# Performance work log

Hardware: AMD Instinct MI355X
Metric: run time of the kernel (lower is better)

The kernel has to match this reference:

```python
import jax, jax.numpy as jnp
import numpy as np

B, F, H, W = 1, 4, 20, 44
P = H * W            # 880 tokens per frame (20*44, from max_attention_size = 15*880)
S = F * P            # 3520 packed tokens
DIM, NH, FFN, OUT = 1536, 12, 6144, 64   # OUT = prod(patch_size)*out_dim = 4*16
HD = DIM // NH       # 128
C = HD // 2          # 64 rotary complex pairs
EPS = 1e-6


def _rope_angles():
    # Wan 3D RoPE: split C pairs as (C-2*(C//3), C//3, C//3) over (frame, h, w)
    cf, ch, cw = C - 2 * (C // 3), C // 3, C // 3
    def tab(n, cp):
        inv = 1.0 / (10000.0 ** (np.arange(cp) / cp))
        return np.outer(np.arange(n), inv)
    af = np.broadcast_to(tab(F, cf)[:, None, None, :], (F, H, W, cf))
    ah = np.broadcast_to(tab(H, ch)[None, :, None, :], (F, H, W, ch))
    aw = np.broadcast_to(tab(W, cw)[None, None, :, :], (F, H, W, cw))
    return np.concatenate([af, ah, aw], -1).reshape(S, C).astype(np.float32)


def setup_inputs() -> dict:
    key = jax.random.key(0)
    ks = jax.random.split(key, 24)
    g = lambda i, shape, s=0.02: jax.random.normal(ks[i], shape, dtype=jnp.float32) * s
    inp = {
        'x': jax.random.normal(ks[0], (B, S, DIM), dtype=jnp.float32),
        'e': g(1, (B, F, 6, DIM), 1.0),
        'e_head': g(2, (B, F, 2, DIM), 1.0),
        'rope_angles': jnp.asarray(_rope_angles()),
        'mod_block': g(3, (1, 6, DIM), 1.0 / float(np.sqrt(DIM))),
        'mod_head': g(4, (1, 2, DIM), 1.0 / float(np.sqrt(DIM))),
        'Wq': g(5, (DIM, DIM)), 'bq': jnp.zeros((DIM,), jnp.float32),
        'Wk': g(6, (DIM, DIM)), 'bk': jnp.zeros((DIM,), jnp.float32),
        'Wv': g(7, (DIM, DIM)), 'bv': jnp.zeros((DIM,), jnp.float32),
        'Wo': g(8, (DIM, DIM)), 'bo': jnp.zeros((DIM,), jnp.float32),
        'wq_norm': jnp.ones((DIM,), jnp.float32),
        'wk_norm': jnp.ones((DIM,), jnp.float32),
        'W1': g(9, (DIM, FFN)), 'b1': jnp.zeros((FFN,), jnp.float32),
        'W2': g(10, (FFN, DIM)), 'b2': jnp.zeros((DIM,), jnp.float32),
        'Wh': g(11, (DIM, OUT)), 'bh': jnp.zeros((OUT,), jnp.float32),
    }
    return inp


def _ln(x):
    # WanLayerNorm without elementwise affine
    m = jnp.mean(x, axis=-1, keepdims=True)
    v = jnp.var(x, axis=-1, keepdims=True)
    return (x - m) * jax.lax.rsqrt(v + EPS)


def _rms(x, w):
    return x * jax.lax.rsqrt(jnp.mean(x * x, axis=-1, keepdims=True) + EPS) * w


def _rope(t, ang):
    # t: [B,S,NH,HD]; adjacent pairs form complex numbers (view_as_complex style)
    tr = t.reshape(B, S, NH, C, 2)
    cos = jnp.cos(ang)[None, :, None, :]
    sin = jnp.sin(ang)[None, :, None, :]
    t0, t1 = tr[..., 0], tr[..., 1]
    return jnp.stack([t0 * cos - t1 * sin, t0 * sin + t1 * cos], -1).reshape(B, S, NH, HD)


def reference(x, e, e_head, rope_angles, mod_block, mod_head,
              Wq, bq, Wk, bk, Wv, bv, Wo, bo, wq_norm, wk_norm,
              W1, b1, W2, b2, Wh, bh):
    # ---- AdaLN modulation split (6-way) ----
    em = mod_block[:, None] + e                      # [B,F,6,DIM]
    e0, e1, e2, e3, e4, e5 = [em[:, :, i][:, :, None, :] for i in range(6)]

    xf = x.reshape(B, F, P, DIM)
    h = (_ln(xf) * (1 + e1) + e0).reshape(B, S, DIM)

    # ---- QK-RMSNorm + RoPE self attention (block-causal, block = one frame) ----
    q = _rope(_rms(h @ Wq + bq, wq_norm).reshape(B, S, NH, HD), rope_angles)
    k = _rope(_rms(h @ Wk + bk, wk_norm).reshape(B, S, NH, HD), rope_angles)
    v = (h @ Wv + bv).reshape(B, S, NH, HD)

    blk = jnp.arange(S) // P
    mask = blk[None, :] <= blk[:, None]              # [S,S] block-causal
    scores = jnp.einsum('bqhd,bkhd->bhqk', q, k) / np.float32(np.sqrt(HD))
    scores = jnp.where(mask[None, None], scores, jnp.float32(-1e30))
    attn = jax.nn.softmax(scores, axis=-1)
    y = jnp.einsum('bhqk,bkhd->bqhd', attn, v).reshape(B, S, DIM) @ Wo + bo

    xf = xf + y.reshape(B, F, P, DIM) * e2

    # ---- FFN with AdaLN modulation ----
    hf = (_ln(xf) * (1 + e4) + e3).reshape(B, S, DIM)
    ff = jax.nn.gelu(hf @ W1 + b1) @ W2 + b2
    xf = xf + ff.reshape(B, F, P, DIM) * e5

    # ---- OutputHead: modulated norm + linear ----
    eh = mod_head[:, None] + e_head                  # [B,F,2,DIM]
    eh0 = eh[:, :, 0][:, :, None, :]
    eh1 = eh[:, :, 1][:, :, None, :]
    out = (_ln(xf) * (1 + eh1) + eh0) @ Wh + bh      # [B,F,P,OUT]
    return out
```

## Files before the change

kernel.cpp:

```cpp
#include <hip/hip_runtime.h>
#include <cstdint>
#include <cstddef>

typedef __bf16 bf16;
typedef __bf16 bf16x2 __attribute__((ext_vector_type(2)));
typedef __bf16 bf16x8 __attribute__((ext_vector_type(8)));
typedef float f32x4 __attribute__((ext_vector_type(4)));
typedef unsigned int u32x4 __attribute__((ext_vector_type(4)));

#define S_TOK 3520
#define S_PAD 3584
#define P_TOK 880
#define NFRM 4
#define DIM 1536
#define NH 12
#define HD 128
#define FFN_D 6144
#define NOUT 64
#define EPSV 1e-6f
#define QSCALE 0.12751743f

__device__ __forceinline__ f32x4 mfma16(bf16x8 a, bf16x8 b, f32x4 c) {
  return __builtin_amdgcn_mfma_f32_16x16x32_bf16(a, b, c, 0, 0, 0);
}

__device__ __forceinline__ void gload_lds16(const bf16* g, bf16* l) {
  __builtin_amdgcn_global_load_lds(
      (const __attribute__((address_space(1))) unsigned int*)g,
      (__attribute__((address_space(3))) unsigned int*)l, 16, 0, 0);
}

__device__ __forceinline__ uint32_t pk2(float lo, float hi) {
  bf16x2 t;
  t[0] = (bf16)lo;
  t[1] = (bf16)hi;
  return __builtin_bit_cast(uint32_t, t);
}

__global__ __launch_bounds__(256) void k_prep(const float* __restrict__ e,
                                              const float* __restrict__ e_head,
                                              const float* __restrict__ mod_block,
                                              const float* __restrict__ mod_head,
                                              float* __restrict__ em,
                                              float* __restrict__ ehm) {
  int i = blockIdx.x * 256 + threadIdx.x;
  if (i < NFRM * 6 * DIM) em[i] = mod_block[i % (6 * DIM)] + e[i];
  int j = i - NFRM * 6 * DIM;
  if (j >= 0 && j < NFRM * 2 * DIM) ehm[j] = mod_head[j % (2 * DIM)] + e_head[j];
}

__global__ __launch_bounds__(256) void k_zero_vpad(bf16* __restrict__ vc) {
  size_t base = ((size_t)blockIdx.x * 28 + 27) * 4096 + 2048 + (size_t)threadIdx.x * 8;
#pragma unroll
  for (int i = 0; i < 8; ++i) vc[base + i] = (bf16)0.f;
}

__global__ __launch_bounds__(256) void k_transpose(const float* __restrict__ W,
                                                   bf16* __restrict__ Wt, int K, int N) {
  __shared__ float tile[32][33];
  int n0 = blockIdx.x * 32, k0 = blockIdx.y * 32;
  int tx = threadIdx.x & 31, ty = threadIdx.x >> 5;
#pragma unroll
  for (int j = 0; j < 4; ++j) {
    int k = k0 + ty * 4 + j;
    float v = (n0 + tx < N) ? W[(size_t)k * N + n0 + tx] : 0.f;
    tile[ty * 4 + j][tx] = v;
  }
  __syncthreads();
#pragma unroll
  for (int j = 0; j < 4; ++j) {
    int n = n0 + ty * 4 + j;
    if (n < N) Wt[(size_t)n * K + k0 + tx] = (bf16)tile[tx][ty * 4 + j];
  }
}

__global__ __launch_bounds__(256) void k_adaln(const float* __restrict__ in,
                                               bf16* __restrict__ out,
                                               const float* __restrict__ e_shift,
                                               const float* __restrict__ e_scale,
                                               int fstride) {
  int tok = blockIdx.x;
  int t = threadIdx.x;
  bf16* orow = out + (size_t)tok * DIM;
  if (tok >= S_TOK) {
#pragma unroll
    for (int i = 0; i < 6; ++i) orow[t * 6 + i] = (bf16)0.f;
    return;
  }
  const float* xrow = in + (size_t)tok * DIM;
  float v[6];
  float s = 0.f, sq = 0.f;
#pragma unroll
  for (int i = 0; i < 6; ++i) {
    v[i] = xrow[t * 6 + i];
    s += v[i];
    sq += v[i] * v[i];
  }
  for (int off = 32; off; off >>= 1) {
    s += __shfl_down(s, off);
    sq += __shfl_down(sq, off);
  }
  __shared__ float red[8];
  int wv = t >> 6, lane = t & 63;
  if (lane == 0) { red[wv] = s; red[4 + wv] = sq; }
  __syncthreads();
  float ts = red[0] + red[1] + red[2] + red[3];
  float tq = red[4] + red[5] + red[6] + red[7];
  float mean = ts * (1.f / DIM);
  float var = tq * (1.f / DIM) - mean * mean;
  float rstd = rsqrtf(var + EPSV);
  int f = tok / P_TOK;
  const float* sh = e_shift + (size_t)f * fstride;
  const float* sc = e_scale + (size_t)f * fstride;
#pragma unroll
  for (int i = 0; i < 6; ++i) {
    int d = t * 6 + i;
    orow[d] = (bf16)((v[i] - mean) * rstd * (1.f + sc[d]) + sh[d]);
  }
}

__global__ __launch_bounds__(256) void k_qkv_post(const float* __restrict__ qkv,
                                                  const float* __restrict__ wqn,
                                                  const float* __restrict__ wkn,
                                                  const float* __restrict__ ang,
                                                  bf16* __restrict__ qb,
                                                  bf16* __restrict__ kb,
                                                  bf16* __restrict__ vc) {
  int s = blockIdx.x;
  int t = threadIdx.x;
  const float* row = qkv + (size_t)s * 3 * DIM;
  float qv[6], kv[6], vv[6];
  float sqq = 0.f, sqk = 0.f;
  int d0 = t * 6;
#pragma unroll
  for (int i = 0; i < 6; ++i) {
    int d = d0 + i;
    qv[i] = row[d];
    kv[i] = row[DIM + d];
    vv[i] = row[2 * DIM + d];
    sqq += qv[i] * qv[i];
    sqk += kv[i] * kv[i];
  }
  float a1 = sqq, a2 = sqk;
  for (int off = 32; off; off >>= 1) {
    a1 += __shfl_down(a1, off);
    a2 += __shfl_down(a2, off);
  }
  __shared__ float red[8];
  int wv = t >> 6, lane = t & 63;
  if (lane == 0) { red[wv] = a1; red[4 + wv] = a2; }
  __syncthreads();
  float tq = red[0] + red[1] + red[2] + red[3];
  float tk = red[4] + red[5] + red[6] + red[7];
  float rq = rsqrtf(tq * (1.f / DIM) + EPSV);
  float rk = rsqrtf(tk * (1.f / DIM) + EPSV);
#pragma unroll
  for (int p = 0; p < 3; ++p) {
    int d = d0 + p * 2;
    int h = d >> 7;
    int hd = d & 127;
    int c = hd >> 1;
    float a = ang[(size_t)s * 64 + c];
    float sa, ca;
    sincosf(a, &sa, &ca);
    float q0 = qv[p * 2] * rq * wqn[d], q1 = qv[p * 2 + 1] * rq * wqn[d + 1];
    float k0 = kv[p * 2] * rk * wkn[d], k1 = kv[p * 2 + 1] * rk * wkn[d + 1];
    size_t base = ((size_t)h * S_TOK + s) * HD + hd;
    qb[base]     = (bf16)((q0 * ca - q1 * sa) * QSCALE);
    qb[base + 1] = (bf16)((q0 * sa + q1 * ca) * QSCALE);
    kb[base]     = (bf16)(k0 * ca - k1 * sa);
    kb[base + 1] = (bf16)(k0 * sa + k1 * ca);
  }
  int f = s / P_TOK;
  int l = s - f * P_TOK;
  int lb = l >> 5, gg = (l >> 3) & 3, r = l & 7;
#pragma unroll
  for (int i = 0; i < 6; ++i) {
    int d = d0 + i;
    int h = d >> 7, hd = d & 127;
    vc[((((size_t)(h * NFRM + f)) * 28 + lb) * 512 + gg * 128 + hd) * 8 + r] = (bf16)vv[i];
  }
}

__global__ __launch_bounds__(320) void k_attn(const bf16* __restrict__ qb,
                                              const bf16* __restrict__ kb,
                                              const bf16* __restrict__ vc,
                                              float* __restrict__ parto,
                                              float* __restrict__ partml) {
  __shared__ __align__(16) bf16 Ks[2][512 * 8];
  __shared__ __align__(16) bf16 Vs[2][512 * 8];
  int h = blockIdx.x / 110;
  int p = blockIdx.x % 110;
  int f = (p < 11) ? 0 : (p < 33) ? 1 : (p < 66) ? 2 : 3;
  int cum = (f == 0) ? 0 : (f == 1) ? 11 : (f == 2) ? 33 : 66;
  int w = p - cum;
  int kc = w / 11;
  int qt = f * 11 + w % 11;
  int slot = blockIdx.x;
  int t = threadIdx.x;
  int wv = t >> 6, lane = t & 63;
  int r16 = lane & 15, g = lane >> 4;
  int q0 = qt * 80 + wv * 16;
  int kv0 = kc * P_TOK;
  const bf16* qbase = qb + ((size_t)h * S_TOK + q0 + r16) * HD + g * 8;
  bf16x8 qf[4];
#pragma unroll
  for (int kk = 0; kk < 4; ++kk) qf[kk] = *(const bf16x8*)(qbase + kk * 32);
  f32x4 acc[8] = {};
  float mrow = -1e30f, lrow = 0.f;
  int src01 = r16 + ((2 * g) & 3) * 16;
  int src23 = src01 + 16;
  bool glo = (g < 2);
  int sB = t + 256;
  int kr0 = t >> 4, kl0 = t & 15;
  int ks0 = (kl0 & 8) | ((kl0 ^ kr0) & 7);
  int kr1 = sB >> 4, kl1 = sB & 15;
  int ks1 = (kl1 & 8) | ((kl1 ^ kr1) & 7);
  const bf16* kh = kb + (size_t)h * S_TOK * HD;
  const bf16* vchunk = vc + ((size_t)(h * NFRM + kc)) * 28 * 4096;
#define STAGE_ATT(buf, jj)                                                  \
  do {                                                                      \
    int kvoj = (jj) * 32;                                                   \
    int gr0 = kv0 + kvoj + kr0; if (gr0 >= S_TOK) gr0 = 0;                  \
    int gr1 = kv0 + kvoj + kr1; if (gr1 >= S_TOK) gr1 = 0;                  \
    gload_lds16(kh + (size_t)gr0 * HD + ks0 * 8, Ks[buf] + t * 8);          \
    gload_lds16(kh + (size_t)gr1 * HD + ks1 * 8, Ks[buf] + sB * 8);         \
    gload_lds16(vchunk + (size_t)(jj) * 4096 + t * 8, Vs[buf] + t * 8);     \
    gload_lds16(vchunk + (size_t)(jj) * 4096 + sB * 8, Vs[buf] + sB * 8);   \
  } while (0)
  const int nsteps = (P_TOK + 31) >> 5;
  if (t < 256) STAGE_ATT(0, 0);
  int cur = 0;
  for (int j = 0; j < nsteps; ++j) {
    int kvo = j * 32;
    if (j + 1 < nsteps) {
      if (t < 256) STAGE_ATT(cur ^ 1, j + 1);
      asm volatile("s_waitcnt vmcnt(4)" ::: "memory");
    } else {
      asm volatile("s_waitcnt vmcnt(0)" ::: "memory");
    }
    __builtin_amdgcn_s_barrier();
    f32x4 st0 = {0.f, 0.f, 0.f, 0.f}, st1 = {0.f, 0.f, 0.f, 0.f};
#pragma unroll
    for (int kk = 0; kk < 4; ++kk) {
      int sl = g + 4 * kk;
      int ss = (sl & 8) | ((sl ^ r16) & 7);
      bf16x8 k0 = *(const bf16x8*)(Ks[cur] + (r16 * 16 + ss) * 8);
      bf16x8 k1 = *(const bf16x8*)(Ks[cur] + ((16 + r16) * 16 + ss) * 8);
      st0 = mfma16(k0, qf[kk], st0);
      st1 = mfma16(k1, qf[kk], st1);
    }
    float hm = (kvo + 16 >= P_TOK) ? -1e30f : 0.f;
    float a0[4], a1[4];
#pragma unroll
    for (int r = 0; r < 4; ++r) {
      a0[r] = st0[r];
      a1[r] = st1[r] + hm;
    }
    float tm = fmaxf(fmaxf(fmaxf(a0[0], a0[1]), fmaxf(a0[2], a0[3])),
                     fmaxf(fmaxf(a1[0], a1[1]), fmaxf(a1[2], a1[3])));
    tm = fmaxf(tm, __shfl_xor(tm, 16));
    tm = fmaxf(tm, __shfl_xor(tm, 32));
    float mn = fmaxf(mrow, tm);
    float p0[4], p1[4], ps = 0.f;
#pragma unroll
    for (int r = 0; r < 4; ++r) {
      p0[r] = exp2f(a0[r] - mn);
      p1[r] = exp2f(a1[r] - mn);
      ps += p0[r] + p1[r];
    }
    float scl = exp2f(mrow - mn);
    mrow = mn;
    lrow = lrow * scl + ps;
    uint32_t A0 = pk2(p0[0], p0[1]), A1 = pk2(p0[2], p0[3]);
    uint32_t B0 = pk2(p1[0], p1[1]), B1 = pk2(p1[2], p1[3]);
    uint32_t sA0 = __shfl(A0, src01), sA1 = __shfl(A1, src01);
    uint32_t sB0 = __shfl(B0, src01), sB1 = __shfl(B1, src01);
    uint32_t tA0 = __shfl(A0, src23), tA1 = __shfl(A1, src23);
    uint32_t tB0 = __shfl(B0, src23), tB1 = __shfl(B1, src23);
    u32x4 wds;
    wds[0] = glo ? sA0 : sB0;
    wds[1] = glo ? sA1 : sB1;
    wds[2] = glo ? tA0 : tB0;
    wds[3] = glo ? tA1 : tB1;
    bf16x8 pb = __builtin_bit_cast(bf16x8, wds);
#pragma unroll
    for (int hb = 0; hb < 8; ++hb) {
      acc[hb][0] *= scl;
      acc[hb][1] *= scl;
      acc[hb][2] *= scl;
      acc[hb][3] *= scl;
    }
    const bf16* vsl = Vs[cur] + (size_t)(g * 128 + r16) * 8;
#pragma unroll
    for (int hb = 0; hb < 8; ++hb) {
      bf16x8 vfr = *(const bf16x8*)(vsl + hb * 128);
      acc[hb] = mfma16(vfr, pb, acc[hb]);
    }
    asm volatile("" ::: "memory");
    __builtin_amdgcn_s_barrier();
    cur ^= 1;
  }
#undef STAGE_ATT
  lrow += __shfl_xor(lrow, 16);
  lrow += __shfl_xor(lrow, 32);
  float* obase = parto + (((size_t)slot * 5 + wv) * 8) * 256;
#pragma unroll
  for (int hb = 0; hb < 8; ++hb) {
    *(f32x4*)(obase + (hb * 64 + lane) * 4) = acc[hb];
  }
  if (g == 0) {
    float* mlb = partml + ((size_t)slot * 5 + wv) * 32;
    mlb[r16] = mrow;
    mlb[16 + r16] = lrow;
  }
}

__global__ __launch_bounds__(256) void k_att_reduce(const float* __restrict__ parto,
                                                    const float* __restrict__ partml,
                                                    bf16* __restrict__ attb) {
  int b = blockIdx.x;
  int h = b / 44, qt = b % 44;
  int f = qt / 11, j = qt % 11;
  int cum = (f == 0) ? 0 : (f == 1) ? 11 : (f == 2) ? 33 : 66;
  int t = threadIdx.x;
  int d = t & 127, half = t >> 7;
  int hb = d >> 4, g = (d >> 2) & 3, r = d & 3;
  int q0 = qt * 80;
  for (int it = 0; it < 40; ++it) {
    int qloc = it + 40 * half;
    int wv = qloc >> 4, r16 = qloc & 15;
    float m[4], l[4];
    float mt = -1e30f;
    for (int kc = 0; kc <= f; ++kc) {
      int slot = h * 110 + cum + kc * 11 + j;
      const float* mlb = partml + ((size_t)slot * 5 + wv) * 32;
      m[kc] = mlb[r16];
      l[kc] = mlb[16 + r16];
      mt = fmaxf(mt, m[kc]);
    }
    float lt = 0.f, o = 0.f;
    for (int kc = 0; kc <= f; ++kc) {
      int slot = h * 110 + cum + kc * 11 + j;
      float wgt = exp2f(m[kc] - mt);
      lt += l[kc] * wgt;
      o += parto[(((size_t)slot * 5 + wv) * 8 + hb) * 256 + (g * 16 + r16) * 4 + r] * wgt;
    }
    attb[(size_t)(q0 + qloc) * DIM + h * HD + d] = (bf16)(o / lt);
  }
}

struct GemmP {
  const bf16* A;
  const bf16* Bt;
  int K;
  int Mtiles;
  int Ntiles;
  int Mreal;
  int mode;
  const float* bias0;
  const float* bias1;
  const float* bias2;
  const float* res;
  const float* emod;
  int e_fstride;
  float* outf;
  bf16* outb;
  int ldo;
};

__global__ __launch_bounds__(256, 3) void k_gemm(GemmP p) {
  int nwg = p.Mtiles * p.Ntiles;
  int bid = blockIdx.x;
  int l = bid;
  if ((nwg & 7) == 0) {
    int cpx = nwg >> 3;
    l = (bid & 7) * cpx + (bid >> 3);
  }
  int bm = l % p.Mtiles;
  int bn = l / p.Mtiles;
  __shared__ __align__(16) bf16 As[3][128 * 32];
  __shared__ __align__(16) bf16 Bs[3][128 * 32];
  int t = threadIdx.x, lane = t & 63, wv = t >> 6;
  int r16 = lane & 15, g = lane >> 4;
  int wr = wv >> 1, wc = wv & 1;
  f32x4 acc[4][4] = {};
  const bf16* Ag = p.A + (size_t)bm * 128 * p.K;
  const bf16* Bg = p.Bt + (size_t)bn * 128 * p.K;
  int c0 = t, c1 = t + 256;
  int row0 = c0 >> 2, off0 = (c0 & 3) * 8;
  int row1 = c1 >> 2, off1 = (c1 & 3) * 8;
#define STAGE(buf, kk)                                                     \
  do {                                                                     \
    gload_lds16(Ag + (size_t)row0 * p.K + (kk) + off0, As[buf] + c0 * 8);  \
    gload_lds16(Ag + (size_t)row1 * p.K + (kk) + off1, As[buf] + c1 * 8);  \
    gload_lds16(Bg + (size_t)row0 * p.K + (kk) + off0, Bs[buf] + c0 * 8);  \
    gload_lds16(Bg + (size_t)row1 * p.K + (kk) + off1, Bs[buf] + c1 * 8);  \
  } while (0)
  const int nt = p.K >> 5;
  STAGE(0, 0);
  STAGE(1, 32);
  int cur = 0;
  for (int tt = 0; tt < nt; ++tt) {
    int rem = nt - 1 - tt;
    if (rem >= 2) {
      int nb = cur + 2;
      if (nb >= 3) nb -= 3;
      STAGE(nb, (tt + 2) * 32);
      asm volatile("s_waitcnt vmcnt(8)" ::: "memory");
    } else if (rem == 1) {
      asm volatile("s_waitcnt vmcnt(4)" ::: "memory");
    } else {
      asm volatile("s_waitcnt vmcnt(0)" ::: "memory");
    }
    __builtin_amdgcn_s_barrier();
    bf16x8 af[4], bfr[4];
#pragma unroll
    for (int mi = 0; mi < 4; ++mi)
      af[mi] = *(const bf16x8*)(As[cur] + (wr * 64 + mi * 16 + r16) * 32 + g * 8);
#pragma unroll
    for (int ni = 0; ni < 4; ++ni)
      bfr[ni] = *(const bf16x8*)(Bs[cur] + (wc * 64 + ni * 16 + r16) * 32 + g * 8);
#pragma unroll
    for (int mi = 0; mi < 4; ++mi)
#pragma unroll
      for (int ni = 0; ni < 4; ++ni)
        acc[mi][ni] = mfma16(af[mi], bfr[ni], acc[mi][ni]);
    asm volatile("" ::: "memory");
    __builtin_amdgcn_s_barrier();
    cur = (cur + 1 == 3) ? 0 : cur + 1;
  }
#undef STAGE
  int mb = bm * 128 + wr * 64, nb0 = bn * 128 + wc * 64;
#pragma unroll
  for (int mi = 0; mi < 4; ++mi) {
#pragma unroll
    for (int ni = 0; ni < 4; ++ni) {
      int col = nb0 + ni * 16 + r16;
#pragma unroll
      for (int r = 0; r < 4; ++r) {
        int row = mb + mi * 16 + 4 * g + r;
        if (row >= p.Mreal) continue;
        float v = acc[mi][ni][r];
        if (p.mode == 0) {
          float b = col < DIM ? p.bias0[col]
                              : (col < 2 * DIM ? p.bias1[col - DIM] : p.bias2[col - 2 * DIM]);
          p.outf[(size_t)row * p.ldo + col] = v + b;
        } else if (p.mode == 1) {
          int fr = row / P_TOK;
          p.outf[(size_t)row * p.ldo + col] =
              p.res[(size_t)row * DIM + col] +
              (v + p.bias0[col]) * p.emod[(size_t)fr * p.e_fstride + col];
        } else if (p.mode == 2) {
          float xg = v + p.bias0[col];
          float gl = 0.5f * xg * (1.f + tanhf(0.7978845608028654f * (xg + 0.044715f * xg * xg * xg)));
          p.outb[(size_t)row * p.ldo + col] = (bf16)gl;
        } else {
          if (col < NOUT) p.outf[(size_t)row * p.ldo + col] = v + p.bias0[col];
        }
      }
    }
  }
}

extern "C" void kernel_launch(void* const* d_in, const int* in_sizes, int n_in,
                              void* d_out, int out_size, void* d_ws, size_t ws_size,
                              hipStream_t stream) {
  const float* x = (const float*)d_in[0];
  const float* e = (const float*)d_in[1];
  const float* e_head = (const float*)d_in[2];
  const float* ang = (const float*)d_in[3];
  const float* mod_block = (const float*)d_in[4];
  const float* mod_head = (const float*)d_in[5];
  const float* Wq = (const float*)d_in[6];
  const float* bq = (const float*)d_in[7];
  const float* Wk = (const float*)d_in[8];
  const float* bk = (const float*)d_in[9];
  const float* Wv = (const float*)d_in[10];
  const float* bv = (const float*)d_in[11];
  const float* Wo = (const float*)d_in[12];
  const float* bo = (const float*)d_in[13];
  const float* wqn = (const float*)d_in[14];
  const float* wkn = (const float*)d_in[15];
  const float* W1 = (const float*)d_in[16];
  const float* b1 = (const float*)d_in[17];
  const float* W2 = (const float*)d_in[18];
  const float* b2 = (const float*)d_in[19];
  const float* Wh = (const float*)d_in[20];
  const float* bh = (const float*)d_in[21];
  float* out = (float*)d_out;
  char* ws = (char*)d_ws;

  size_t WT_QKV = 0;
  size_t WT_O = WT_QKV + (size_t)3 * DIM * DIM * 2;
  size_t W1T = WT_O + (size_t)DIM * DIM * 2;
  size_t W2T = W1T + (size_t)FFN_D * DIM * 2;
  size_t WHT = W2T + (size_t)DIM * FFN_D * 2;
  size_t EMOFF = WHT + (size_t)128 * DIM * 2;
  size_t EHOFF = EMOFF + (size_t)NFRM * 6 * DIM * 4;
  size_t HB = EHOFF + (size_t)NFRM * 2 * DIM * 4;
  size_t CQKV = HB + (size_t)S_PAD * DIM * 2;
  size_t DQB = CQKV + (size_t)S_TOK * 3 * DIM * 4;
  size_t EATT = DQB + (size_t)3 * NH * S_TOK * HD * 2;
  size_t GXF2 = EATT + (size_t)S_PAD * DIM * 2;
  size_t END = GXF2 + (size_t)S_TOK * DIM * 4;
  if (ws_size < END) return;

  bf16* wtqkv = (bf16*)(ws + WT_QKV);
  bf16* wto = (bf16*)(ws + WT_O);
  bf16* w1t = (bf16*)(ws + W1T);
  bf16* w2t = (bf16*)(ws + W2T);
  bf16* wht = (bf16*)(ws + WHT);
  float* em = (float*)(ws + EMOFF);
  float* ehm = (float*)(ws + EHOFF);
  bf16* hb = (bf16*)(ws + HB);
  float* qkvf = (float*)(ws + CQKV);
  bf16* ffb = (bf16*)(ws + CQKV);
  float* parto = (float*)(ws + CQKV);
  float* partml = parto + (size_t)1320 * 5 * 8 * 256;
  bf16* qbp = (bf16*)(ws + DQB);
  bf16* kbp = qbp + (size_t)NH * S_TOK * HD;
  bf16* vcp = kbp + (size_t)NH * S_TOK * HD;
  float* xf3 = (float*)(ws + DQB);
  bf16* attb = (bf16*)(ws + EATT);
  float* xf2 = (float*)(ws + GXF2);

  k_prep<<<(NFRM * 8 * DIM) / 256, 256, 0, stream>>>(e, e_head, mod_block, mod_head, em, ehm);
  k_zero_vpad<<<NH * NFRM, 256, 0, stream>>>(vcp);

  k_transpose<<<dim3(48, 48), 256, 0, stream>>>(Wq, wtqkv, DIM, DIM);
  k_transpose<<<dim3(48, 48), 256, 0, stream>>>(Wk, wtqkv + (size_t)DIM * DIM, DIM, DIM);
  k_transpose<<<dim3(48, 48), 256, 0, stream>>>(Wv, wtqkv + (size_t)2 * DIM * DIM, DIM, DIM);
  k_transpose<<<dim3(48, 48), 256, 0, stream>>>(Wo, wto, DIM, DIM);
  k_transpose<<<dim3(192, 48), 256, 0, stream>>>(W1, w1t, DIM, FFN_D);
  k_transpose<<<dim3(48, 192), 256, 0, stream>>>(W2, w2t, FFN_D, DIM);
  k_transpose<<<dim3(2, 48), 256, 0, stream>>>(Wh, wht, DIM, NOUT);
  hipMemsetAsync(ws + WHT + (size_t)NOUT * DIM * 2, 0, (size_t)(128 - NOUT) * DIM * 2, stream);
  hipMemsetAsync(ws + EATT + (size_t)S_TOK * DIM * 2, 0, (size_t)(S_PAD - S_TOK) * DIM * 2, stream);

  k_adaln<<<S_PAD, 256, 0, stream>>>(x, hb, em, em + DIM, 6 * DIM);

  GemmP g0{};
  g0.A = hb; g0.Bt = wtqkv; g0.K = DIM; g0.Mtiles = 28; g0.Ntiles = 36; g0.Mreal = S_TOK;
  g0.mode = 0; g0.bias0 = bq; g0.bias1 = bk; g0.bias2 = bv; g0.outf = qkvf; g0.ldo = 3 * DIM;
  k_gemm<<<28 * 36, 256, 0, stream>>>(g0);

  k_qkv_post<<<S_TOK, 256, 0, stream>>>(qkvf, wqn, wkn, ang, qbp, kbp, vcp);

  k_attn<<<NH * 110, 320, 0, stream>>>(qbp, kbp, vcp, parto, partml);
  k_att_reduce<<<NH * 44, 256, 0, stream>>>(parto, partml, attb);

  GemmP g1{};
  g1.A = attb; g1.Bt = wto; g1.K = DIM; g1.Mtiles = 28; g1.Ntiles = 12; g1.Mreal = S_TOK;
  g1.mode = 1; g1.bias0 = bo; g1.res = x; g1.emod = em + 2 * DIM; g1.e_fstride = 6 * DIM;
  g1.outf = xf2; g1.ldo = DIM;
  k_gemm<<<28 * 12, 256, 0, stream>>>(g1);

  k_adaln<<<S_PAD, 256, 0, stream>>>(xf2, hb, em + 3 * DIM, em + 4 * DIM, 6 * DIM);

  GemmP g2{};
  g2.A = hb; g2.Bt = w1t; g2.K = DIM; g2.Mtiles = 28; g2.Ntiles = 48; g2.Mreal = S_TOK;
  g2.mode = 2; g2.bias0 = b1; g2.outb = ffb; g2.ldo = FFN_D;
  k_gemm<<<28 * 48, 256, 0, stream>>>(g2);
  hipMemsetAsync(ws + CQKV + (size_t)S_TOK * FFN_D * 2, 0, (size_t)(S_PAD - S_TOK) * FFN_D * 2, stream);

  GemmP g3{};
  g3.A = ffb; g3.Bt = w2t; g3.K = FFN_D; g3.Mtiles = 28; g3.Ntiles = 12; g3.Mreal = S_TOK;
  g3.mode = 1; g3.bias0 = b2; g3.res = xf2; g3.emod = em + 5 * DIM; g3.e_fstride = 6 * DIM;
  g3.outf = xf3; g3.ldo = DIM;
  k_gemm<<<28 * 12, 256, 0, stream>>>(g3);

  k_adaln<<<S_PAD, 256, 0, stream>>>(xf3, hb, ehm, ehm + DIM, 2 * DIM);

  GemmP g4{};
  g4.A = hb; g4.Bt = wht; g4.K = DIM; g4.Mtiles = 28; g4.Ntiles = 1; g4.Mreal = S_TOK;
  g4.mode = 4; g4.bias0 = bh; g4.outf = out; g4.ldo = NOUT;
  k_gemm<<<28, 256, 0, stream>>>(g4);
}
```

Measured before the change: 803.0 us.

## Use 256x256-tile 512-thread GEMM kernel for QKV and FFN-up projections

Adds a new GEMM kernel with 256x256 output tiles, 8 waves per block, double-buffered swizzled LDS staging, XCD-aware block remapping and MFMA priority hints. It is used for the QKV projection and the first FFN matmul with GELU in place of the 128-tile kernel. The larger tiles raise arithmetic intensity and cut global reloads of A and B. In exchange it uses 128KB of LDS, which limits blocks per CU, and fewer blocks (252 and 336) may leave CUs underused or give wave-quantization tails.

```diff
diff --git a/kernel.cpp b/kernel.cpp
--- a/kernel.cpp
+++ b/kernel.cpp
@@ -347,6 +347,124 @@
       o += parto[(((size_t)slot * 5 + wv) * 8 + hb) * 256 + (g * 16 + r16) * 4 + r] * wgt;
     }
     attb[(size_t)(q0 + qloc) * DIM + h * HD + d] = (bf16)(o / lt);
+  }
+}
+
+struct Gemm256P {
+  const bf16* A;
+  const bf16* Bt;
+  int K;
+  int Mtiles;
+  int Ntiles;
+  int Mreal;
+  int mode;
+  const float* bias0;
+  const float* bias1;
+  const float* bias2;
+  float* outf;
+  bf16* outb;
+  int ldo;
+};
+
+__global__ __launch_bounds__(512, 2) void k_gemm256(Gemm256P p) {
+  int nwg = p.Mtiles * p.Ntiles;
+  int bid = blockIdx.x;
+  int xq = nwg >> 3, xr = nwg & 7;
+  int xcd = bid & 7, jj = bid >> 3;
+  int wg = (xcd < xr ? xcd * (xq + 1) : xr * (xq + 1) + (xcd - xr) * xq) + jj;
+  int bm = wg % p.Mtiles;
+  int bn = wg / p.Mtiles;
+  __shared__ __align__(16) bf16 Asl[2][256 * 64];
+  __shared__ __align__(16) bf16 Bsl[2][256 * 64];
+  int t = threadIdx.x, lane = t & 63, wv = t >> 6;
+  int r16 = lane & 15, g = lane >> 4;
+  int wr = wv >> 2, wc = wv & 3;
+  f32x4 acc[8][4] = {};
+  const bf16* Ag = p.A + (size_t)bm * 256 * p.K;
+  const bf16* Bg = p.Bt + (size_t)bn * 256 * p.K;
+  int r7 = r16 & 7;
+#define STAGE256(buf, kt)                                                        \
+  do {                                                                           \
+    int k0s = (kt) * 64;                                                         \
+    _Pragma("unroll") for (int o = 0; o < 4; ++o) {                              \
+      int b = o * 512 + t;                                                       \
+      int rw = b >> 3;                                                           \
+      int cb = (b & 7) ^ (rw & 7);                                               \
+      gload_lds16(Ag + (size_t)rw * p.K + k0s + cb * 8, Asl[buf] + b * 8);       \
+    }                                                                            \
+    _Pragma("unroll") for (int o = 0; o < 4; ++o) {                              \
+      int b = o * 512 + t;                                                       \
+      int rw = b >> 3;                                                           \
+      int cb = (b & 7) ^ (rw & 7);                                               \
+      gload_lds16(Bg + (size_t)rw * p.K + k0s + cb * 8, Bsl[buf] + b * 8);       \
+    }                                                                            \
+  } while (0)
+  const int nt = p.K >> 6;
+  STAGE256(0, 0);
+  int cur = 0;
+  for (int tt = 0; tt < nt; ++tt) {
+    if (tt + 1 < nt) {
+      STAGE256(cur ^ 1, tt + 1);
+      asm volatile("s_waitcnt vmcnt(8)" ::: "memory");
+    } else {
+      asm volatile("s_waitcnt vmcnt(0)" ::: "memory");
+    }
+    __builtin_amdgcn_s_barrier();
+    const bf16* Ac = Asl[cur];
+    const bf16* Bc = Bsl[cur];
+#pragma unroll
+    for (int q = 0; q < 4; ++q) {
+      int mb0 = (q >> 1) * 4, nb0 = (q & 1) * 2;
+      bf16x8 af[4][2], bfr[2][2];
+#pragma unroll
+      for (int mi = 0; mi < 4; ++mi)
+#pragma unroll
+        for (int kk = 0; kk < 2; ++kk)
+          af[mi][kk] = *(const bf16x8*)(Ac + (size_t)(wr * 128 + (mb0 + mi) * 16 + r16) * 64 +
+                                        (((kk * 4 + g) ^ r7) * 8));
+#pragma unroll
+      for (int ni = 0; ni < 2; ++ni)
+#pragma unroll
+        for (int kk = 0; kk < 2; ++kk)
+          bfr[ni][kk] = *(const bf16x8*)(Bc + (size_t)(wc * 64 + (nb0 + ni) * 16 + r16) * 64 +
+                                         (((kk * 4 + g) ^ r7) * 8));
+      __builtin_amdgcn_s_setprio(1);
+#pragma unroll
+      for (int mi = 0; mi < 4; ++mi)
+#pragma unroll
+        for (int ni = 0; ni < 2; ++ni)
+#pragma unroll
+          for (int kk = 0; kk < 2; ++kk)
+            acc[mb0 + mi][nb0 + ni] = mfma16(af[mi][kk], bfr[ni][kk], acc[mb0 + mi][nb0 + ni]);
+      __builtin_amdgcn_s_setprio(0);
+    }
+    asm volatile("" ::: "memory");
+    __builtin_amdgcn_s_barrier();
+    cur ^= 1;
+  }
+#undef STAGE256
+  int mbase = bm * 256 + wr * 128, nbase = bn * 256 + wc * 64;
+#pragma unroll
+  for (int mi = 0; mi < 8; ++mi) {
+#pragma unroll
+    for (int ni = 0; ni < 4; ++ni) {
+      int col = nbase + ni * 16 + r16;
+#pragma unroll
+      for (int r = 0; r < 4; ++r) {
+        int row = mbase + mi * 16 + 4 * g + r;
+        if (row >= p.Mreal) continue;
+        float v = acc[mi][ni][r];
+        if (p.mode == 0) {
+          float b = col < DIM ? p.bias0[col]
+                              : (col < 2 * DIM ? p.bias1[col - DIM] : p.bias2[col - 2 * DIM]);
+          p.outf[(size_t)row * p.ldo + col] = v + b;
+        } else {
+          float xg = v + p.bias0[col];
+          float gl = 0.5f * xg * (1.f + tanhf(0.7978845608028654f * (xg + 0.044715f * xg * xg * xg)));
+          p.outb[(size_t)row * p.ldo + col] = (bf16)gl;
+        }
+      }
+    }
   }
 }
 
@@ -540,10 +658,10 @@
 
   k_adaln<<<S_PAD, 256, 0, stream>>>(x, hb, em, em + DIM, 6 * DIM);
 
-  GemmP g0{};
-  g0.A = hb; g0.Bt = wtqkv; g0.K = DIM; g0.Mtiles = 28; g0.Ntiles = 36; g0.Mreal = S_TOK;
-  g0.mode = 0; g0.bias0 = bq; g0.bias1 = bk; g0.bias2 = bv; g0.outf = qkvf; g0.ldo = 3 * DIM;
-  k_gemm<<<28 * 36, 256, 0, stream>>>(g0);
+  Gemm256P q0{};
+  q0.A = hb; q0.Bt = wtqkv; q0.K = DIM; q0.Mtiles = 14; q0.Ntiles = 18; q0.Mreal = S_TOK;
+  q0.mode = 0; q0.bias0 = bq; q0.bias1 = bk; q0.bias2 = bv; q0.outf = qkvf; q0.ldo = 3 * DIM;
+  k_gemm256<<<14 * 18, 512, 0, stream>>>(q0);
 
   k_qkv_post<<<S_TOK, 256, 0, stream>>>(qkvf, wqn, wkn, ang, qbp, kbp, vcp);
 
@@ -558,10 +676,10 @@
 
   k_adaln<<<S_PAD, 256, 0, stream>>>(xf2, hb, em + 3 * DIM, em + 4 * DIM, 6 * DIM);
 
-  GemmP g2{};
-  g2.A = hb; g2.Bt = w1t; g2.K = DIM; g2.Mtiles = 28; g2.Ntiles = 48; g2.Mreal = S_TOK;
-  g2.mode = 2; g2.bias0 = b1; g2.outb = ffb; g2.ldo = FFN_D;
-  k_gemm<<<28 * 48, 256, 0, stream>>>(g2);
+  Gemm256P q2{};
+  q2.A = hb; q2.Bt = w1t; q2.K = DIM; q2.Mtiles = 14; q2.Ntiles = 24; q2.Mreal = S_TOK;
+  q2.mode = 2; q2.bias0 = b1; q2.outb = ffb; q2.ldo = FFN_D;
+  k_gemm256<<<14 * 24, 512, 0, stream>>>(q2);
   hipMemsetAsync(ws + CQKV + (size_t)S_TOK * FFN_D * 2, 0, (size_t)(S_PAD - S_TOK) * FFN_D * 2, stream);
 
   GemmP g3{};
```

After: 817.1 us. No clear change (+1.8%).

## Rework GEMM kernel: 512 threads, BK=64 double buffer, XOR-swizzled LDS, XCD-aware mapping

Applied to the files above, without the earlier changes.

Restructures the shared GEMM kernel to use 8 waves per block with 64x32 warp tiles, a K-step of 64 with two LDS buffers instead of three buffers of 32, and an XOR swizzle on LDS columns to avoid bank conflicts. The block-to-tile mapping is changed to an XCD-aware remap that also handles grid sizes not divisible by 8, and s_setprio brackets the MFMA section. The aim is fewer barriers per K and better LDS bandwidth, at the cost of a shallower prefetch pipeline and a larger LDS footprint per block.

```diff
diff --git a/kernel.cpp b/kernel.cpp
--- a/kernel.cpp
+++ b/kernel.cpp
@@ -369,77 +369,81 @@
   int ldo;
 };
 
-__global__ __launch_bounds__(256, 3) void k_gemm(GemmP p) {
+__global__ __launch_bounds__(512, 4) void k_gemm(GemmP p) {
   int nwg = p.Mtiles * p.Ntiles;
   int bid = blockIdx.x;
-  int l = bid;
-  if ((nwg & 7) == 0) {
-    int cpx = nwg >> 3;
-    l = (bid & 7) * cpx + (bid >> 3);
-  }
-  int bm = l % p.Mtiles;
-  int bn = l / p.Mtiles;
-  __shared__ __align__(16) bf16 As[3][128 * 32];
-  __shared__ __align__(16) bf16 Bs[3][128 * 32];
+  int xq = nwg >> 3, xr = nwg & 7;
+  int xcd = bid & 7, jj = bid >> 3;
+  int wg = (xcd < xr ? xcd * (xq + 1) : xr * (xq + 1) + (xcd - xr) * xq) + jj;
+  int bm = wg % p.Mtiles;
+  int bn = wg / p.Mtiles;
+  __shared__ __align__(16) bf16 Asl[2][128 * 64];
+  __shared__ __align__(16) bf16 Bsl[2][128 * 64];
   int t = threadIdx.x, lane = t & 63, wv = t >> 6;
   int r16 = lane & 15, g = lane >> 4;
-  int wr = wv >> 1, wc = wv & 1;
-  f32x4 acc[4][4] = {};
+  int s7 = r16 & 7;
+  int wr = wv >> 2, wc = wv & 3;
+  f32x4 acc[4][2] = {};
   const bf16* Ag = p.A + (size_t)bm * 128 * p.K;
   const bf16* Bg = p.Bt + (size_t)bn * 128 * p.K;
-  int c0 = t, c1 = t + 256;
-  int row0 = c0 >> 2, off0 = (c0 & 3) * 8;
-  int row1 = c1 >> 2, off1 = (c1 & 3) * 8;
-#define STAGE(buf, kk)                                                     \
-  do {                                                                     \
-    gload_lds16(Ag + (size_t)row0 * p.K + (kk) + off0, As[buf] + c0 * 8);  \
-    gload_lds16(Ag + (size_t)row1 * p.K + (kk) + off1, As[buf] + c1 * 8);  \
-    gload_lds16(Bg + (size_t)row0 * p.K + (kk) + off0, Bs[buf] + c0 * 8);  \
-    gload_lds16(Bg + (size_t)row1 * p.K + (kk) + off1, Bs[buf] + c1 * 8);  \
+  int b0 = t, b1 = t + 512;
+  int rw0 = b0 >> 3, cb0 = (b0 & 7) ^ (rw0 & 7);
+  int rw1 = b1 >> 3, cb1 = (b1 & 7) ^ (rw1 & 7);
+#define STAGE(d, kt)                                                          \
+  do {                                                                        \
+    int k0s = (kt) * 64;                                                      \
+    gload_lds16(Ag + (size_t)rw0 * p.K + k0s + cb0 * 8, Asl[d] + b0 * 8);     \
+    gload_lds16(Ag + (size_t)rw1 * p.K + k0s + cb1 * 8, Asl[d] + b1 * 8);     \
+    gload_lds16(Bg + (size_t)rw0 * p.K + k0s + cb0 * 8, Bsl[d] + b0 * 8);     \
+    gload_lds16(Bg + (size_t)rw1 * p.K + k0s + cb1 * 8, Bsl[d] + b1 * 8);     \
   } while (0)
-  const int nt = p.K >> 5;
+  const int nt = p.K >> 6;
   STAGE(0, 0);
-  STAGE(1, 32);
   int cur = 0;
   for (int tt = 0; tt < nt; ++tt) {
-    int rem = nt - 1 - tt;
-    if (rem >= 2) {
-      int nb = cur + 2;
-      if (nb >= 3) nb -= 3;
-      STAGE(nb, (tt + 2) * 32);
-      asm volatile("s_waitcnt vmcnt(8)" ::: "memory");
-    } else if (rem == 1) {
+    if (tt + 1 < nt) {
+      STAGE(cur ^ 1, tt + 1);
       asm volatile("s_waitcnt vmcnt(4)" ::: "memory");
     } else {
       asm volatile("s_waitcnt vmcnt(0)" ::: "memory");
     }
     __builtin_amdgcn_s_barrier();
-    bf16x8 af[4], bfr[4];
+    bf16x8 af[4][2], bfr[2][2];
 #pragma unroll
     for (int mi = 0; mi < 4; ++mi)
-      af[mi] = *(const bf16x8*)(As[cur] + (wr * 64 + mi * 16 + r16) * 32 + g * 8);
-#pragma unroll
-    for (int ni = 0; ni < 4; ++ni)
-      bfr[ni] = *(const bf16x8*)(Bs[cur] + (wc * 64 + ni * 16 + r16) * 32 + g * 8);
+#pragma unroll
+      for (int kk = 0; kk < 2; ++kk)
+        af[mi][kk] = *(const bf16x8*)(Asl[cur] + (size_t)(wr * 64 + mi * 16 + r16) * 64 +
+                                      (((kk * 4 + g) ^ s7) * 8));
+#pragma unroll
+    for (int ni = 0; ni < 2; ++ni)
+#pragma unroll
+      for (int kk = 0; kk < 2; ++kk)
+        bfr[ni][kk] = *(const bf16x8*)(Bsl[cur] + (size_t)(wc * 32 + ni * 16 + r16) * 64 +
+                                       (((kk * 4 + g) ^ s7) * 8));
+    __builtin_amdgcn_s_setprio(1);
 #pragma unroll
     for (int mi = 0; mi < 4; ++mi)
 #pragma unroll
-      for (int ni = 0; ni < 4; ++ni)
-        acc[mi][ni] = mfma16(af[mi], bfr[ni], acc[mi][ni]);
+      for (int ni = 0; ni < 2; ++ni)
+#pragma unroll
+        for (int kk = 0; kk < 2; ++kk)
+          acc[mi][ni] = mfma16(af[mi][kk], bfr[ni][kk], acc[mi][ni]);
+    __builtin_amdgcn_s_setprio(0);
     asm volatile("" ::: "memory");
     __builtin_amdgcn_s_barrier();
-    cur = (cur + 1 == 3) ? 0 : cur + 1;
+    cur ^= 1;
   }
 #undef STAGE
-  int mb = bm * 128 + wr * 64, nb0 = bn * 128 + wc * 64;
+  int mbase = bm * 128 + wr * 64, nbase = bn * 128 + wc * 32;
 #pragma unroll
   for (int mi = 0; mi < 4; ++mi) {
 #pragma unroll
-    for (int ni = 0; ni < 4; ++ni) {
-      int col = nb0 + ni * 16 + r16;
+    for (int ni = 0; ni < 2; ++ni) {
+      int col = nbase + ni * 16 + r16;
 #pragma unroll
       for (int r = 0; r < 4; ++r) {
-        int row = mb + mi * 16 + 4 * g + r;
+        int row = mbase + mi * 16 + 4 * g + r;
         if (row >= p.Mreal) continue;
         float v = acc[mi][ni][r];
         if (p.mode == 0) {
@@ -543,7 +547,7 @@
   GemmP g0{};
   g0.A = hb; g0.Bt = wtqkv; g0.K = DIM; g0.Mtiles = 28; g0.Ntiles = 36; g0.Mreal = S_TOK;
   g0.mode = 0; g0.bias0 = bq; g0.bias1 = bk; g0.bias2 = bv; g0.outf = qkvf; g0.ldo = 3 * DIM;
-  k_gemm<<<28 * 36, 256, 0, stream>>>(g0);
+  k_gemm<<<28 * 36, 512, 0, stream>>>(g0);
 
   k_qkv_post<<<S_TOK, 256, 0, stream>>>(qkvf, wqn, wkn, ang, qbp, kbp, vcp);
 
@@ -554,26 +558,26 @@
   g1.A = attb; g1.Bt = wto; g1.K = DIM; g1.Mtiles = 28; g1.Ntiles = 12; g1.Mreal = S_TOK;
   g1.mode = 1; g1.bias0 = bo; g1.res = x; g1.emod = em + 2 * DIM; g1.e_fstride = 6 * DIM;
   g1.outf = xf2; g1.ldo = DIM;
-  k_gemm<<<28 * 12, 256, 0, stream>>>(g1);
+  k_gemm<<<28 * 12, 512, 0, stream>>>(g1);
 
   k_adaln<<<S_PAD, 256, 0, stream>>>(xf2, hb, em + 3 * DIM, em + 4 * DIM, 6 * DIM);
 
   GemmP g2{};
   g2.A = hb; g2.Bt = w1t; g2.K = DIM; g2.Mtiles = 28; g2.Ntiles = 48; g2.Mreal = S_TOK;
   g2.mode = 2; g2.bias0 = b1; g2.outb = ffb; g2.ldo = FFN_D;
-  k_gemm<<<28 * 48, 256, 0, stream>>>(g2);
+  k_gemm<<<28 * 48, 512, 0, stream>>>(g2);
   hipMemsetAsync(ws + CQKV + (size_t)S_TOK * FFN_D * 2, 0, (size_t)(S_PAD - S_TOK) * FFN_D * 2, stream);
 
   GemmP g3{};
   g3.A = ffb; g3.Bt = w2t; g3.K = FFN_D; g3.Mtiles = 28; g3.Ntiles = 12; g3.Mreal = S_TOK;
   g3.mode = 1; g3.bias0 = b2; g3.res = xf2; g3.emod = em + 5 * DIM; g3.e_fstride = 6 * DIM;
   g3.outf = xf3; g3.ldo = DIM;
-  k_gemm<<<28 * 12, 256, 0, stream>>>(g3);
+  k_gemm<<<28 * 12, 512, 0, stream>>>(g3);
 
   k_adaln<<<S_PAD, 256, 0, stream>>>(xf3, hb, ehm, ehm + DIM, 2 * DIM);
 
   GemmP g4{};
   g4.A = hb; g4.Bt = wht; g4.K = DIM; g4.Mtiles = 28; g4.Ntiles = 1; g4.Mreal = S_TOK;
   g4.mode = 4; g4.bias0 = bh; g4.outf = out; g4.ldo = NOUT;
-  k_gemm<<<28, 256, 0, stream>>>(g4);
-}
+  k_gemm<<<28, 512, 0, stream>>>(g4);
+}
```

New measurement: 689.7 us. 14.1% less time.
